# Kernel optimization log

Hardware: AMD Instinct MI355X
Metric: run time of the kernel (lower is better)

## Reference

```python
import jax, jax.numpy as jnp
import numpy as np

B, T, D, H = 4, 2048, 1024, 16
HD = D // H


def setup_inputs() -> dict:
    key = jax.random.key(0)
    ks = jax.random.split(key, 4)
    x = jax.random.normal(ks[0], (B, T, D), dtype=jnp.float32)
    # causal lower-triangular mask, broadcastable to [B, H, T, T]
    mask = jnp.tril(jnp.ones((T, T), dtype=bool))[None, None, :, :]
    w_qkv = jax.random.normal(ks[1], (D, 3 * D), dtype=jnp.float32) * (1.0 / np.sqrt(D))
    b_qkv = jnp.zeros((3 * D,), dtype=jnp.float32)
    w_out = jax.random.normal(ks[2], (D, D), dtype=jnp.float32) * (1.0 / np.sqrt(D))
    b_out = jnp.zeros((D,), dtype=jnp.float32)
    return {"x": x, "mask": mask, "w_qkv": w_qkv, "b_qkv": b_qkv,
            "w_out": w_out, "b_out": b_out}


def reference(x, mask, w_qkv, b_qkv, w_out, b_out):
    Bx, Tx, C = x.shape
    qkv = x @ w_qkv + b_qkv                       # [B, T, 3D]
    q, k, v = jnp.split(qkv, 3, axis=-1)
    # [B, T, H, hd] -> [B, H, T, hd]
    q = q.reshape(Bx, Tx, H, HD).transpose(0, 2, 1, 3)
    k = k.reshape(Bx, Tx, H, HD).transpose(0, 2, 1, 3)
    v = v.reshape(Bx, Tx, H, HD).transpose(0, 2, 1, 3)
    scale = 1.0 / np.sqrt(HD).astype(np.float32)
    att = jnp.einsum('bhqd,bhkd->bhqk', q, k) * scale   # [B, H, T, T]
    att = jnp.where(mask, att, -jnp.inf)
    att = jax.nn.softmax(att, axis=-1)
    y = jnp.einsum('bhqk,bhkd->bhqd', att, v)            # [B, H, T, hd]
    y = y.transpose(0, 2, 1, 3).reshape(Bx, Tx, C)
    return y @ w_out + b_out
```

## Files before the change

kernel.cpp:

```cpp
#include <hip/hip_runtime.h>


typedef unsigned short u16;
typedef unsigned int u32;
typedef __attribute__((ext_vector_type(8))) short short8;
typedef __attribute__((ext_vector_type(4))) float f32x4;

#define MASKV (-1e30f)
#define SCLOG 0.1803368801111444f

__device__ __forceinline__ u16 f2bf(float f) {
  union { float f; u32 u; } x; x.f = f;
  u32 r = x.u + 0x7FFFu + ((x.u >> 16) & 1u);
  return (u16)(r >> 16);
}

__device__ __forceinline__ void async16(const u16* g, u16* l) {
  __builtin_amdgcn_global_load_lds((__attribute__((address_space(1))) void*)g,
                                   (__attribute__((address_space(3))) void*)l,
                                   16, 0, 0);
}

__global__ void cvt_x_kernel(const float* __restrict__ x, u16* __restrict__ xb) {
  size_t i = ((size_t)blockIdx.x * 256 + threadIdx.x) * 4;
  float4 v = *(const float4*)(x + i);
  uint2 o;
  o.x = (u32)f2bf(v.x) | ((u32)f2bf(v.y) << 16);
  o.y = (u32)f2bf(v.z) | ((u32)f2bf(v.w) << 16);
  *(uint2*)(xb + i) = o;
}

__global__ void cvt_tr_kernel(const float* __restrict__ src, u16* __restrict__ dst,
                              int K, int N) {
  __shared__ float tile[32][33];
  int n0 = blockIdx.x * 32, k0 = blockIdx.y * 32;
  int tx = threadIdx.x & 31, ty = threadIdx.x >> 5;
  #pragma unroll
  for (int r = ty; r < 32; r += 8)
    tile[r][tx] = src[(size_t)(k0 + r) * N + n0 + tx];
  __syncthreads();
  #pragma unroll
  for (int r = ty; r < 32; r += 8)
    dst[(size_t)(n0 + r) * K + k0 + tx] = f2bf(tile[tx][r]);
}

template<bool BF16OUT>
__global__ __launch_bounds__(256) void gemm_bt(const u16* __restrict__ A,
                                               const u16* __restrict__ Bt,
                                               const float* __restrict__ bias,
                                               void* __restrict__ Cv, int N) {
  constexpr int K = 1024;
  __shared__ alignas(16) u16 As[128 * 32];
  __shared__ alignas(16) u16 Bs[128 * 32];
  const int t = threadIdx.x;
  const int w = t >> 6, lane = t & 63, quad = lane >> 4, l15 = lane & 15;
  const int m0 = blockIdx.y * 128, n0 = blockIdx.x * 128;
  const int wm = (w >> 1) * 64, wn = (w & 1) * 64;

  size_t gA[2], gB[2];
  int lds_st[2];
  #pragma unroll
  for (int ii = 0; ii < 2; ii++) {
    const int row = w * 32 + ii * 16 + (lane >> 2);
    const int db = (lane & 3) ^ (row & 3);
    gA[ii] = (size_t)(m0 + row) * K + db * 8;
    gB[ii] = (size_t)(n0 + row) * K + db * 8;
    lds_st[ii] = (w * 32 + ii * 16) * 32 + lane * 8;
  }
  const int fsw = (quad ^ (l15 & 3)) << 3;

  f32x4 acc[4][4];
  #pragma unroll
  for (int i = 0; i < 4; i++)
    #pragma unroll
    for (int j = 0; j < 4; j++)
      acc[i][j] = (f32x4){0.f, 0.f, 0.f, 0.f};

  for (int k0 = 0; k0 < K; k0 += 32) {
    __syncthreads();
    async16(A + gA[0] + k0, As + lds_st[0]);
    async16(A + gA[1] + k0, As + lds_st[1]);
    async16(Bt + gB[0] + k0, Bs + lds_st[0]);
    async16(Bt + gB[1] + k0, Bs + lds_st[1]);
    __syncthreads();
    short8 af[4], bf[4];
    #pragma unroll
    for (int i = 0; i < 4; i++)
      af[i] = *(const short8*)(As + (wm + i * 16 + l15) * 32 + fsw);
    #pragma unroll
    for (int j = 0; j < 4; j++)
      bf[j] = *(const short8*)(Bs + (wn + j * 16 + l15) * 32 + fsw);
    #pragma unroll
    for (int i = 0; i < 4; i++)
      #pragma unroll
      for (int j = 0; j < 4; j++)
        acc[i][j] = __builtin_amdgcn_mfma_f32_16x16x32_bf16(af[i], bf[j], acc[i][j], 0, 0, 0);
  }
  #pragma unroll
  for (int j = 0; j < 4; j++) {
    const int col = n0 + wn + j * 16 + l15;
    const float bv = bias[col];
    #pragma unroll
    for (int i = 0; i < 4; i++) {
      const int row = m0 + wm + i * 16 + quad * 4;
      #pragma unroll
      for (int r = 0; r < 4; r++) {
        float v = acc[i][j][r] + bv;
        if (BF16OUT) ((u16*)Cv)[(size_t)(row + r) * N + col] = f2bf(v);
        else         ((float*)Cv)[(size_t)(row + r) * N + col] = v;
      }
    }
  }
}

__global__ __launch_bounds__(256) void flash_kernel(const u16* __restrict__ qkv,
                                                    u16* __restrict__ attn) {
  constexpr int T = 2048, N3 = 3072;
  __shared__ alignas(16) u16 Ks[2][64 * 64];
  __shared__ alignas(16) u16 VsT[2][64 * 64];
  __shared__ alignas(16) u16 Ps[4][32 * 64];
  const int t = threadIdx.x;
  const int w = t >> 6, lane = t & 63, quad = lane >> 4, l15 = lane & 15;
  const int bh = blockIdx.x, b = bh >> 4, h = bh & 15;
  const u16* base = qkv + (size_t)b * T * N3 + h * 64;
  const u16* Kg = base + 1024;
  const u16* Vg = base + 2048;

  size_t gK[2];
  int ldsK[2];
  #pragma unroll
  for (int ii = 0; ii < 2; ii++) {
    const int key0 = w * 16 + ii * 8;
    const int key = key0 + (lane >> 3);
    const int db = ((lane & 7) ^ (key0 >> 3) ^ (lane >> 3)) & 7;
    gK[ii] = (size_t)key * N3 + db * 8;
    ldsK[ii] = key0 * 64 + lane * 8;
  }
  const int vkey = w * 8 + (lane >> 3);
  const int vchunk = lane & 7;
  const size_t gV = (size_t)vkey * N3 + vchunk * 8;

  short8 onesf;
  #pragma unroll
  for (int j = 0; j < 8; j++) onesf[j] = (short)0x3F80;

  #pragma unroll 1
  for (int half = 0; half < 2; half++) {
    const int qt = half ? (int)blockIdx.y : 15 - (int)blockIdx.y;
    const int q0 = qt * 128;
    const int qw = q0 + w * 32;
    const int ktmax = 2 * qt + 1;

    short8 qf[2][2];
    #pragma unroll
    for (int mi = 0; mi < 2; mi++)
      #pragma unroll
      for (int kc = 0; kc < 2; kc++)
        qf[mi][kc] = *(const short8*)(base + (size_t)(qw + mi * 16 + l15) * N3 + kc * 32 + quad * 8);

    f32x4 o[2][4], lac[2];
    #pragma unroll
    for (int mi = 0; mi < 2; mi++) {
      lac[mi] = (f32x4){0.f, 0.f, 0.f, 0.f};
      #pragma unroll
      for (int dt = 0; dt < 4; dt++) o[mi][dt] = (f32x4){0.f, 0.f, 0.f, 0.f};
    }

    async16(Kg + gK[0], &Ks[0][ldsK[0]]);
    async16(Kg + gK[1], &Ks[0][ldsK[1]]);
    {
      int4 vp0 = *(const int4*)(Vg + gV);
      int4 vp1 = *(const int4*)(Vg + gV + (size_t)32 * N3);
      union { int4 v; u16 u[8]; } uv;
      #pragma unroll
      for (int rd = 0; rd < 2; rd++) {
        uv.v = rd ? vp1 : vp0;
        const int kb = w + 4 * rd, ko = lane >> 3;
        #pragma unroll
        for (int j = 0; j < 8; j++)
          VsT[0][(vchunk * 8 + j) * 64 + (((kb ^ vchunk ^ j) & 7) << 3) + ko] = uv.u[j];
      }
    }

    int cur = 0;
    for (int kt = 0; kt <= ktmax; ++kt) {
      __syncthreads();
      const bool live = (kt * 64 <= qw + 31);
      const u16* Kc = Ks[cur];
      const u16* Vc = VsT[cur];
      short8 kf[4][2];
      if (live) {
        #pragma unroll
        for (int nt = 0; nt < 4; nt++) {
          const int kx = (nt * 2 + (l15 >> 3)) ^ (l15 & 7);
          #pragma unroll
          for (int ks = 0; ks < 2; ks++)
            kf[nt][ks] = *(const short8*)(Kc + (nt * 16 + l15) * 64 +
                                          ((((ks * 4 + quad) ^ kx) & 7) << 3));
        }
      }
      int4 vp0, vp1;
      if (kt < ktmax) {
        const size_t koff = (size_t)(kt + 1) * 64 * N3;
        async16(Kg + koff + gK[0], &Ks[cur ^ 1][ldsK[0]]);
        async16(Kg + koff + gK[1], &Ks[cur ^ 1][ldsK[1]]);
        vp0 = *(const int4*)(Vg + koff + gV);
        vp1 = *(const int4*)(Vg + koff + gV + (size_t)32 * N3);
      }
      if (live) {
        u16* pw = Ps[w];
        const bool needMask = (kt * 64 + 63 > qw);
        #pragma unroll
        for (int mi = 0; mi < 2; mi++) {
          f32x4 s[4];
          #pragma unroll
          for (int nt = 0; nt < 4; nt++) s[nt] = (f32x4){0.f, 0.f, 0.f, 0.f};
          #pragma unroll
          for (int nt = 0; nt < 4; nt++)
            #pragma unroll
            for (int kc = 0; kc < 2; kc++)
              s[nt] = __builtin_amdgcn_mfma_f32_16x16x32_bf16(qf[mi][kc], kf[nt][kc], s[nt], 0, 0, 0);
          if (needMask) {
            #pragma unroll
            for (int r = 0; r < 4; r++) {
              const int row = qw + mi * 16 + quad * 4 + r;
              #pragma unroll
              for (int nt = 0; nt < 4; nt++) {
                const int col = kt * 64 + nt * 16 + l15;
                if (col > row) s[nt][r] = MASKV;
              }
            }
          }
          #pragma unroll
          for (int nt = 0; nt < 4; nt++) {
            const int lc = nt * 2 + (l15 >> 3);
            #pragma unroll
            for (int r = 0; r < 4; r++) {
              const int rl = mi * 16 + quad * 4 + r;
              const float p = __builtin_amdgcn_exp2f(fminf(s[nt][r], 400.f) * SCLOG);
              union { float f; u32 u; } pc; pc.f = p;
              const int fp_ = (rl ^ (rl >> 1)) & 7;
              pw[rl * 64 + (((lc ^ fp_) & 7) << 3) + (l15 & 7)] = (u16)(pc.u >> 16);
            }
          }
        }
        const int fpr = (l15 ^ (l15 >> 1)) & 7;
        #pragma unroll
        for (int ks = 0; ks < 2; ks++) {
          const int cb = ks * 4 + quad;
          const int ph = (cb ^ fpr) & 7;
          short8 pf0 = *(const short8*)(pw + l15 * 64 + (ph << 3));
          short8 pf1 = *(const short8*)(pw + (16 + l15) * 64 + (ph << 3));
          #pragma unroll
          for (int dt = 0; dt < 4; dt++) {
            const int vx = (dt * 2 + (l15 >> 3)) ^ (l15 & 7);
            short8 vf = *(const short8*)(Vc + (dt * 16 + l15) * 64 + (((cb ^ vx) & 7) << 3));
            o[0][dt] = __builtin_amdgcn_mfma_f32_16x16x32_bf16(pf0, vf, o[0][dt], 0, 0, 0);
            o[1][dt] = __builtin_amdgcn_mfma_f32_16x16x32_bf16(pf1, vf, o[1][dt], 0, 0, 0);
          }
          lac[0] = __builtin_amdgcn_mfma_f32_16x16x32_bf16(pf0, onesf, lac[0], 0, 0, 0);
          lac[1] = __builtin_amdgcn_mfma_f32_16x16x32_bf16(pf1, onesf, lac[1], 0, 0, 0);
        }
      }
      if (kt < ktmax) {
        u16* Vn = (u16*)VsT[cur ^ 1];
        union { int4 v; u16 u[8]; } uv;
        #pragma unroll
        for (int rd = 0; rd < 2; rd++) {
          uv.v = rd ? vp1 : vp0;
          const int kb = w + 4 * rd, ko = lane >> 3;
          #pragma unroll
          for (int j = 0; j < 8; j++)
            Vn[(vchunk * 8 + j) * 64 + (((kb ^ vchunk ^ j) & 7) << 3) + ko] = uv.u[j];
        }
      }
      cur ^= 1;
    }

    #pragma unroll
    for (int mi = 0; mi < 2; mi++)
      #pragma unroll
      for (int r = 0; r < 4; r++) {
        const float invl = 1.0f / lac[mi][r];
        const int row = qw + mi * 16 + quad * 4 + r;
        const size_t off = (size_t)(b * T + row) * 1024 + h * 64;
        #pragma unroll
        for (int dt = 0; dt < 4; dt++)
          attn[off + dt * 16 + l15] = f2bf(o[mi][dt][r] * invl);
      }
  }
}

extern "C" void kernel_launch(void* const* d_in, const int* in_sizes, int n_in,
                              void* d_out, int out_size, void* d_ws, size_t ws_size,
                              hipStream_t stream) {
  (void)in_sizes; (void)n_in; (void)out_size; (void)ws_size;
  const float* x     = (const float*)d_in[0];
  const float* w_qkv = (const float*)d_in[2];
  const float* b_qkv = (const float*)d_in[3];
  const float* w_out = (const float*)d_in[4];
  const float* b_out = (const float*)d_in[5];
  float* out = (float*)d_out;

  char* ws = (char*)d_ws;
  u16* xb    = (u16*)(ws);
  u16* wqkvT = (u16*)(ws + 16777216);
  u16* woutT = (u16*)(ws + 23068672);
  u16* qkvb  = (u16*)(ws + 25165824);
  u16* attnb = (u16*)(ws + 75497472);

  cvt_x_kernel<<<8192, 256, 0, stream>>>(x, xb);
  cvt_tr_kernel<<<dim3(96, 32), 256, 0, stream>>>(w_qkv, wqkvT, 1024, 3072);
  cvt_tr_kernel<<<dim3(32, 32), 256, 0, stream>>>(w_out, woutT, 1024, 1024);
  gemm_bt<true ><<<dim3(24, 64), 256, 0, stream>>>(xb, wqkvT, b_qkv, qkvb, 3072);
  flash_kernel<<<dim3(64, 8), 256, 0, stream>>>(qkvb, attnb);
  gemm_bt<false><<<dim3(8, 64), 256, 0, stream>>>(attnb, woutT, b_out, out, 1024);
}
```

Measured before the change: 329.0 us.

## Pre-transpose V and rewrite flash kernel with 32x32 MFMA, register-resident P

Adds a separate kernel that writes V transposed per head into workspace, so the attention kernel reads K and V^T straight from global memory with no LDS staging or double buffering. The flash kernel now gives each wave its own 32-query strip and uses 32x32x16 MFMAs computing S^T, so P goes from registers into the PV MFMA through a cross-half shuffle instead of an LDS round trip. Row sums are accumulated in scalar registers rather than with a ones-MFMA. Each block now covers one 128-query tile on a grid twice as large, and output is staged through LDS for coalesced stores. The tradeoff is an extra launch plus a write and reread of V, and more reliance on L2 for K/V reuse across waves.

```diff
diff --git a/kernel.cpp b/kernel.cpp
--- a/kernel.cpp
+++ b/kernel.cpp
@@ -5,9 +5,10 @@
 typedef unsigned int u32;
 typedef __attribute__((ext_vector_type(8))) short short8;
 typedef __attribute__((ext_vector_type(4))) float f32x4;
-
+typedef __attribute__((ext_vector_type(16))) float f32x16;
+
+#define SCLOG 0.1803368801111444f
 #define MASKV (-1e30f)
-#define SCLOG 0.1803368801111444f
 
 __device__ __forceinline__ u16 f2bf(float f) {
   union { float f; u32 u; } x; x.f = f;
@@ -113,181 +114,148 @@
   }
 }
 
+__global__ __launch_bounds__(256) void vt_kernel(const u16* __restrict__ qkv,
+                                                 u16* __restrict__ vt) {
+  __shared__ alignas(16) u16 L[64 * 64];
+  const int t = threadIdx.x;
+  const int w = t >> 6, lane = t & 63;
+  const int bh = blockIdx.y;
+  const int b = bh >> 4, h = bh & 15;
+  const int t0 = blockIdx.x * 64;
+  const u16* Vg = qkv + (size_t)b * 2048 * 3072 + 2048 + h * 64;
+  const int vkey = w * 8 + (lane >> 3);
+  const int vchunk = lane & 7;
+  int4 v0 = *(const int4*)(Vg + (size_t)(t0 + vkey) * 3072 + vchunk * 8);
+  int4 v1 = *(const int4*)(Vg + (size_t)(t0 + vkey + 32) * 3072 + vchunk * 8);
+  union { int4 v; u16 u[8]; } uv;
+  #pragma unroll
+  for (int rd = 0; rd < 2; rd++) {
+    uv.v = rd ? v1 : v0;
+    const int kb = w + 4 * rd, ko = lane >> 3;
+    #pragma unroll
+    for (int j = 0; j < 8; j++)
+      L[(vchunk * 8 + j) * 64 + (((kb ^ vchunk ^ j) & 7) << 3) + ko] = uv.u[j];
+  }
+  __syncthreads();
+  const int d = t >> 2;
+  #pragma unroll
+  for (int gg = 0; gg < 2; gg++) {
+    const int g = (t & 3) * 2 + gg;
+    const int phys = (g ^ (d >> 3) ^ (d & 7)) & 7;
+    int4 val = *(const int4*)(L + d * 64 + phys * 8);
+    *(int4*)(vt + ((size_t)bh * 64 + d) * 2048 + t0 + g * 8) = val;
+  }
+}
+
 __global__ __launch_bounds__(256) void flash_kernel(const u16* __restrict__ qkv,
+                                                    const u16* __restrict__ vt,
                                                     u16* __restrict__ attn) {
   constexpr int T = 2048, N3 = 3072;
-  __shared__ alignas(16) u16 Ks[2][64 * 64];
-  __shared__ alignas(16) u16 VsT[2][64 * 64];
-  __shared__ alignas(16) u16 Ps[4][32 * 64];
+  __shared__ alignas(16) u16 Ob[4][32 * 64];
   const int t = threadIdx.x;
-  const int w = t >> 6, lane = t & 63, quad = lane >> 4, l15 = lane & 15;
+  const int w = t >> 6, lane = t & 63;
+  const int col = lane & 31, half = lane >> 5;
   const int bh = blockIdx.x, b = bh >> 4, h = bh & 15;
+  const int s = (15 - (int)blockIdx.y) * 4 + w;
+  const int s32 = s * 32;
   const u16* base = qkv + (size_t)b * T * N3 + h * 64;
   const u16* Kg = base + 1024;
-  const u16* Vg = base + 2048;
-
-  size_t gK[2];
-  int ldsK[2];
-  #pragma unroll
-  for (int ii = 0; ii < 2; ii++) {
-    const int key0 = w * 16 + ii * 8;
-    const int key = key0 + (lane >> 3);
-    const int db = ((lane & 7) ^ (key0 >> 3) ^ (lane >> 3)) & 7;
-    gK[ii] = (size_t)key * N3 + db * 8;
-    ldsK[ii] = key0 * 64 + lane * 8;
-  }
-  const int vkey = w * 8 + (lane >> 3);
-  const int vchunk = lane & 7;
-  const size_t gV = (size_t)vkey * N3 + vchunk * 8;
-
-  short8 onesf;
-  #pragma unroll
-  for (int j = 0; j < 8; j++) onesf[j] = (short)0x3F80;
-
-  #pragma unroll 1
-  for (int half = 0; half < 2; half++) {
-    const int qt = half ? (int)blockIdx.y : 15 - (int)blockIdx.y;
-    const int q0 = qt * 128;
-    const int qw = q0 + w * 32;
-    const int ktmax = 2 * qt + 1;
-
-    short8 qf[2][2];
-    #pragma unroll
-    for (int mi = 0; mi < 2; mi++)
-      #pragma unroll
-      for (int kc = 0; kc < 2; kc++)
-        qf[mi][kc] = *(const short8*)(base + (size_t)(qw + mi * 16 + l15) * N3 + kc * 32 + quad * 8);
-
-    f32x4 o[2][4], lac[2];
-    #pragma unroll
-    for (int mi = 0; mi < 2; mi++) {
-      lac[mi] = (f32x4){0.f, 0.f, 0.f, 0.f};
-      #pragma unroll
-      for (int dt = 0; dt < 4; dt++) o[mi][dt] = (f32x4){0.f, 0.f, 0.f, 0.f};
-    }
-
-    async16(Kg + gK[0], &Ks[0][ldsK[0]]);
-    async16(Kg + gK[1], &Ks[0][ldsK[1]]);
-    {
-      int4 vp0 = *(const int4*)(Vg + gV);
-      int4 vp1 = *(const int4*)(Vg + gV + (size_t)32 * N3);
-      union { int4 v; u16 u[8]; } uv;
-      #pragma unroll
-      for (int rd = 0; rd < 2; rd++) {
-        uv.v = rd ? vp1 : vp0;
-        const int kb = w + 4 * rd, ko = lane >> 3;
+  const u16* Vt = vt + (size_t)bh * 64 * 2048;
+
+  short8 qf[4];
+  {
+    const u16* qrow = base + (size_t)(s32 + col) * N3 + half * 8;
+    #pragma unroll
+    for (int kk = 0; kk < 4; kk++)
+      qf[kk] = *(const short8*)(qrow + kk * 16);
+  }
+
+  f32x16 o[2];
+  o[0] = (f32x16)(0.f);
+  o[1] = (f32x16)(0.f);
+  float l_acc = 0.f;
+
+  const int ntiles = (s >> 1) + 1;
+  for (int kt = 0; kt < ntiles; ++kt) {
+    #pragma unroll
+    for (int st = 0; st < 2; st++) {
+      const int keybase = kt * 64 + st * 32;
+      if (keybase > s32) break;
+      const u16* krow = Kg + (size_t)(keybase + col) * N3 + half * 8;
+      short8 kf[4];
+      #pragma unroll
+      for (int kk = 0; kk < 4; kk++)
+        kf[kk] = *(const short8*)(krow + kk * 16);
+      f32x16 S = (f32x16)(0.f);
+      #pragma unroll
+      for (int kk = 0; kk < 4; kk++)
+        S = __builtin_amdgcn_mfma_f32_32x32x16_bf16(kf[kk], qf[kk], S, 0, 0, 0);
+      union { f32x16 v; u32 u[16]; float f[16]; } su;
+      su.v = S;
+      if (keybase == s32) {
         #pragma unroll
-        for (int j = 0; j < 8; j++)
-          VsT[0][(vchunk * 8 + j) * 64 + (((kb ^ vchunk ^ j) & 7) << 3) + ko] = uv.u[j];
-      }
-    }
-
-    int cur = 0;
-    for (int kt = 0; kt <= ktmax; ++kt) {
-      __syncthreads();
-      const bool live = (kt * 64 <= qw + 31);
-      const u16* Kc = Ks[cur];
-      const u16* Vc = VsT[cur];
-      short8 kf[4][2];
-      if (live) {
+        for (int i = 0; i < 16; i++) {
+          const int kl = (i & 3) + 8 * (i >> 2) + 4 * half;
+          if (kl > col) su.f[i] = MASKV;
+        }
+      }
+      #pragma unroll
+      for (int i = 0; i < 16; i++) {
+        const float p = __builtin_amdgcn_exp2f(fminf(su.f[i], 240.f) * SCLOG);
+        union { float f; u32 u; } pc; pc.f = p;
+        su.u[i] = pc.u;
+        union { u32 u; float f; } tr; tr.u = pc.u & 0xFFFF0000u;
+        l_acc += tr.f;
+      }
+      u32 pk[8], xp[8];
+      #pragma unroll
+      for (int bq = 0; bq < 4; bq++)
         #pragma unroll
-        for (int nt = 0; nt < 4; nt++) {
-          const int kx = (nt * 2 + (l15 >> 3)) ^ (l15 & 7);
-          #pragma unroll
-          for (int ks = 0; ks < 2; ks++)
-            kf[nt][ks] = *(const short8*)(Kc + (nt * 16 + l15) * 64 +
-                                          ((((ks * 4 + quad) ^ kx) & 7) << 3));
+        for (int c = 0; c < 2; c++)
+          pk[bq * 2 + c] = __builtin_amdgcn_perm(su.u[(bq << 2) + (c << 1) + 1],
+                                                 su.u[(bq << 2) + (c << 1)], 0x07060302u);
+      #pragma unroll
+      for (int i = 0; i < 8; i++)
+        xp[i] = (u32)__shfl_xor((int)pk[i], 32, 64);
+      #pragma unroll
+      for (int cc = 0; cc < 2; cc++) {
+        union { u32 d[4]; short8 s8; } pf;
+        pf.d[0] = half ? xp[4 * cc + 2] : pk[4 * cc];
+        pf.d[1] = half ? xp[4 * cc + 3] : pk[4 * cc + 1];
+        pf.d[2] = half ? pk[4 * cc + 2] : xp[4 * cc];
+        pf.d[3] = half ? pk[4 * cc + 3] : xp[4 * cc + 1];
+        #pragma unroll
+        for (int dt = 0; dt < 2; dt++) {
+          const short8 vf = *(const short8*)(Vt + (size_t)(dt * 32 + col) * 2048 +
+                                             keybase + cc * 16 + half * 8);
+          o[dt] = __builtin_amdgcn_mfma_f32_32x32x16_bf16(vf, pf.s8, o[dt], 0, 0, 0);
         }
       }
-      int4 vp0, vp1;
-      if (kt < ktmax) {
-        const size_t koff = (size_t)(kt + 1) * 64 * N3;
-        async16(Kg + koff + gK[0], &Ks[cur ^ 1][ldsK[0]]);
-        async16(Kg + koff + gK[1], &Ks[cur ^ 1][ldsK[1]]);
-        vp0 = *(const int4*)(Vg + koff + gV);
-        vp1 = *(const int4*)(Vg + koff + gV + (size_t)32 * N3);
-      }
-      if (live) {
-        u16* pw = Ps[w];
-        const bool needMask = (kt * 64 + 63 > qw);
-        #pragma unroll
-        for (int mi = 0; mi < 2; mi++) {
-          f32x4 s[4];
-          #pragma unroll
-          for (int nt = 0; nt < 4; nt++) s[nt] = (f32x4){0.f, 0.f, 0.f, 0.f};
-          #pragma unroll
-          for (int nt = 0; nt < 4; nt++)
-            #pragma unroll
-            for (int kc = 0; kc < 2; kc++)
-              s[nt] = __builtin_amdgcn_mfma_f32_16x16x32_bf16(qf[mi][kc], kf[nt][kc], s[nt], 0, 0, 0);
-          if (needMask) {
-            #pragma unroll
-            for (int r = 0; r < 4; r++) {
-              const int row = qw + mi * 16 + quad * 4 + r;
-              #pragma unroll
-              for (int nt = 0; nt < 4; nt++) {
-                const int col = kt * 64 + nt * 16 + l15;
-                if (col > row) s[nt][r] = MASKV;
-              }
-            }
-          }
-          #pragma unroll
-          for (int nt = 0; nt < 4; nt++) {
-            const int lc = nt * 2 + (l15 >> 3);
-            #pragma unroll
-            for (int r = 0; r < 4; r++) {
-              const int rl = mi * 16 + quad * 4 + r;
-              const float p = __builtin_amdgcn_exp2f(fminf(s[nt][r], 400.f) * SCLOG);
-              union { float f; u32 u; } pc; pc.f = p;
-              const int fp_ = (rl ^ (rl >> 1)) & 7;
-              pw[rl * 64 + (((lc ^ fp_) & 7) << 3) + (l15 & 7)] = (u16)(pc.u >> 16);
-            }
-          }
-        }
-        const int fpr = (l15 ^ (l15 >> 1)) & 7;
-        #pragma unroll
-        for (int ks = 0; ks < 2; ks++) {
-          const int cb = ks * 4 + quad;
-          const int ph = (cb ^ fpr) & 7;
-          short8 pf0 = *(const short8*)(pw + l15 * 64 + (ph << 3));
-          short8 pf1 = *(const short8*)(pw + (16 + l15) * 64 + (ph << 3));
-          #pragma unroll
-          for (int dt = 0; dt < 4; dt++) {
-            const int vx = (dt * 2 + (l15 >> 3)) ^ (l15 & 7);
-            short8 vf = *(const short8*)(Vc + (dt * 16 + l15) * 64 + (((cb ^ vx) & 7) << 3));
-            o[0][dt] = __builtin_amdgcn_mfma_f32_16x16x32_bf16(pf0, vf, o[0][dt], 0, 0, 0);
-            o[1][dt] = __builtin_amdgcn_mfma_f32_16x16x32_bf16(pf1, vf, o[1][dt], 0, 0, 0);
-          }
-          lac[0] = __builtin_amdgcn_mfma_f32_16x16x32_bf16(pf0, onesf, lac[0], 0, 0, 0);
-          lac[1] = __builtin_amdgcn_mfma_f32_16x16x32_bf16(pf1, onesf, lac[1], 0, 0, 0);
-        }
-      }
-      if (kt < ktmax) {
-        u16* Vn = (u16*)VsT[cur ^ 1];
-        union { int4 v; u16 u[8]; } uv;
-        #pragma unroll
-        for (int rd = 0; rd < 2; rd++) {
-          uv.v = rd ? vp1 : vp0;
-          const int kb = w + 4 * rd, ko = lane >> 3;
-          #pragma unroll
-          for (int j = 0; j < 8; j++)
-            Vn[(vchunk * 8 + j) * 64 + (((kb ^ vchunk ^ j) & 7) << 3) + ko] = uv.u[j];
-        }
-      }
-      cur ^= 1;
-    }
-
-    #pragma unroll
-    for (int mi = 0; mi < 2; mi++)
-      #pragma unroll
-      for (int r = 0; r < 4; r++) {
-        const float invl = 1.0f / lac[mi][r];
-        const int row = qw + mi * 16 + quad * 4 + r;
-        const size_t off = (size_t)(b * T + row) * 1024 + h * 64;
-        #pragma unroll
-        for (int dt = 0; dt < 4; dt++)
-          attn[off + dt * 16 + l15] = f2bf(o[mi][dt][r] * invl);
-      }
+    }
+  }
+
+  const float l_tot = l_acc + (float)__shfl_xor(l_acc, 32, 64);
+  const float inv = 1.0f / l_tot;
+
+  u16* buf = Ob[w];
+  #pragma unroll
+  for (int dt = 0; dt < 2; dt++)
+    #pragma unroll
+    for (int i = 0; i < 16; i++) {
+      const int d = dt * 32 + (i & 3) + 8 * (i >> 2) + 4 * half;
+      buf[col * 64 + ((((d >> 3) ^ (col & 7)) & 7) << 3) + (d & 7)] = f2bf(o[dt][i] * inv);
+    }
+  __syncthreads();
+  {
+    const int qr = lane >> 1;
+    const size_t orow = (size_t)(b * T + s32 + qr) * 1024 + h * 64;
+    #pragma unroll
+    for (int ccs = 0; ccs < 4; ccs++) {
+      const int c = (lane & 1) * 4 + ccs;
+      const int phys = (c ^ (qr & 7)) & 7;
+      int4 val = *(const int4*)(buf + qr * 64 + phys * 8);
+      *(int4*)(attn + orow + c * 8) = val;
+    }
   }
 }
 
@@ -307,12 +275,14 @@
   u16* wqkvT = (u16*)(ws + 16777216);
   u16* woutT = (u16*)(ws + 23068672);
   u16* qkvb  = (u16*)(ws + 25165824);
-  u16* attnb = (u16*)(ws + 75497472);
+  u16* vtb   = (u16*)(ws + 75497472);
+  u16* attnb = xb;
 
   cvt_x_kernel<<<8192, 256, 0, stream>>>(x, xb);
   cvt_tr_kernel<<<dim3(96, 32), 256, 0, stream>>>(w_qkv, wqkvT, 1024, 3072);
   cvt_tr_kernel<<<dim3(32, 32), 256, 0, stream>>>(w_out, woutT, 1024, 1024);
   gemm_bt<true ><<<dim3(24, 64), 256, 0, stream>>>(xb, wqkvT, b_qkv, qkvb, 3072);
-  flash_kernel<<<dim3(64, 8), 256, 0, stream>>>(qkvb, attnb);
+  vt_kernel<<<dim3(32, 64), 256, 0, stream>>>(qkvb, vtb);
+  flash_kernel<<<dim3(64, 16), 256, 0, stream>>>(qkvb, vtb, attnb);
   gemm_bt<false><<<dim3(8, 64), 256, 0, stream>>>(attnb, woutT, b_out, out, 1024);
 }
```

Result: slower. 354.2 us (+7.7%).

## Split flash attention into 64-row query tiles with one block per tile

Applied to the files above, without the earlier changes.

The flash kernel goes from 512 blocks, each handling two paired 128-row query tiles (a long and a short one, for causal balance), to 2048 blocks that each handle one 64-row tile, with 16 rows per wave. This raises parallelism and occupancy through smaller per-thread register and LDS footprints, and removes the per-wave dead-tile 'live' checks. The cost is reloading each K/V tile for more query tiles, which doubles K/V traffic, and relying on the scheduler to balance uneven causal work. The attention output buffer now reuses the x bf16 workspace, and the exp clamp is lowered.

```diff
diff --git a/kernel.cpp b/kernel.cpp
--- a/kernel.cpp
+++ b/kernel.cpp
@@ -118,10 +118,13 @@
   constexpr int T = 2048, N3 = 3072;
   __shared__ alignas(16) u16 Ks[2][64 * 64];
   __shared__ alignas(16) u16 VsT[2][64 * 64];
-  __shared__ alignas(16) u16 Ps[4][32 * 64];
+  __shared__ alignas(16) u16 Ps[4][16 * 64];
   const int t = threadIdx.x;
   const int w = t >> 6, lane = t & 63, quad = lane >> 4, l15 = lane & 15;
   const int bh = blockIdx.x, b = bh >> 4, h = bh & 15;
+  const int qt = 31 - (int)blockIdx.y;
+  const int qw = qt * 64 + w * 16;
+
   const u16* base = qkv + (size_t)b * T * N3 + h * 64;
   const u16* Kg = base + 1024;
   const u16* Vg = base + 2048;
@@ -144,33 +147,104 @@
   #pragma unroll
   for (int j = 0; j < 8; j++) onesf[j] = (short)0x3F80;
 
-  #pragma unroll 1
-  for (int half = 0; half < 2; half++) {
-    const int qt = half ? (int)blockIdx.y : 15 - (int)blockIdx.y;
-    const int q0 = qt * 128;
-    const int qw = q0 + w * 32;
-    const int ktmax = 2 * qt + 1;
-
-    short8 qf[2][2];
-    #pragma unroll
-    for (int mi = 0; mi < 2; mi++)
+  short8 qf[2];
+  #pragma unroll
+  for (int kc = 0; kc < 2; kc++)
+    qf[kc] = *(const short8*)(base + (size_t)(qw + l15) * N3 + kc * 32 + quad * 8);
+
+  f32x4 o[4], lac;
+  lac = (f32x4){0.f, 0.f, 0.f, 0.f};
+  #pragma unroll
+  for (int dt = 0; dt < 4; dt++) o[dt] = (f32x4){0.f, 0.f, 0.f, 0.f};
+
+  async16(Kg + gK[0], &Ks[0][ldsK[0]]);
+  async16(Kg + gK[1], &Ks[0][ldsK[1]]);
+  {
+    int4 vp0 = *(const int4*)(Vg + gV);
+    int4 vp1 = *(const int4*)(Vg + gV + (size_t)32 * N3);
+    union { int4 v; u16 u[8]; } uv;
+    #pragma unroll
+    for (int rd = 0; rd < 2; rd++) {
+      uv.v = rd ? vp1 : vp0;
+      const int kb = w + 4 * rd, ko = lane >> 3;
+      #pragma unroll
+      for (int j = 0; j < 8; j++)
+        VsT[0][(vchunk * 8 + j) * 64 + (((kb ^ vchunk ^ j) & 7) << 3) + ko] = uv.u[j];
+    }
+  }
+
+  int cur = 0;
+  for (int kt = 0; kt <= qt; ++kt) {
+    __syncthreads();
+    const u16* Kc = Ks[cur];
+    const u16* Vc = VsT[cur];
+    u16* pw = Ps[w];
+    short8 kf[4][2];
+    #pragma unroll
+    for (int nt = 0; nt < 4; nt++) {
+      const int kx = (nt * 2 + (l15 >> 3)) ^ (l15 & 7);
+      #pragma unroll
+      for (int ks = 0; ks < 2; ks++)
+        kf[nt][ks] = *(const short8*)(Kc + (nt * 16 + l15) * 64 +
+                                      ((((ks * 4 + quad) ^ kx) & 7) << 3));
+    }
+    int4 vp0, vp1;
+    if (kt < qt) {
+      const size_t koff = (size_t)(kt + 1) * 64 * N3;
+      async16(Kg + koff + gK[0], &Ks[cur ^ 1][ldsK[0]]);
+      async16(Kg + koff + gK[1], &Ks[cur ^ 1][ldsK[1]]);
+      vp0 = *(const int4*)(Vg + koff + gV);
+      vp1 = *(const int4*)(Vg + koff + gV + (size_t)32 * N3);
+    }
+
+    f32x4 s[4];
+    #pragma unroll
+    for (int nt = 0; nt < 4; nt++) s[nt] = (f32x4){0.f, 0.f, 0.f, 0.f};
+    #pragma unroll
+    for (int nt = 0; nt < 4; nt++)
       #pragma unroll
       for (int kc = 0; kc < 2; kc++)
-        qf[mi][kc] = *(const short8*)(base + (size_t)(qw + mi * 16 + l15) * N3 + kc * 32 + quad * 8);
-
-    f32x4 o[2][4], lac[2];
-    #pragma unroll
-    for (int mi = 0; mi < 2; mi++) {
-      lac[mi] = (f32x4){0.f, 0.f, 0.f, 0.f};
-      #pragma unroll
-      for (int dt = 0; dt < 4; dt++) o[mi][dt] = (f32x4){0.f, 0.f, 0.f, 0.f};
-    }
-
-    async16(Kg + gK[0], &Ks[0][ldsK[0]]);
-    async16(Kg + gK[1], &Ks[0][ldsK[1]]);
-    {
-      int4 vp0 = *(const int4*)(Vg + gV);
-      int4 vp1 = *(const int4*)(Vg + gV + (size_t)32 * N3);
+        s[nt] = __builtin_amdgcn_mfma_f32_16x16x32_bf16(qf[kc], kf[nt][kc], s[nt], 0, 0, 0);
+
+    if (kt == qt) {
+      #pragma unroll
+      for (int r = 0; r < 4; r++) {
+        const int row = qw + quad * 4 + r;
+        #pragma unroll
+        for (int nt = 0; nt < 4; nt++) {
+          const int col = kt * 64 + nt * 16 + l15;
+          if (col > row) s[nt][r] = MASKV;
+        }
+      }
+    }
+    #pragma unroll
+    for (int nt = 0; nt < 4; nt++) {
+      const int lc = nt * 2 + (l15 >> 3);
+      #pragma unroll
+      for (int r = 0; r < 4; r++) {
+        const int rl = quad * 4 + r;
+        const float p = __builtin_amdgcn_exp2f(fminf(s[nt][r], 240.f) * SCLOG);
+        union { float f; u32 u; } pc; pc.f = p;
+        const int fp_ = (rl ^ (rl >> 1)) & 7;
+        pw[rl * 64 + (((lc ^ fp_) & 7) << 3) + (l15 & 7)] = (u16)(pc.u >> 16);
+      }
+    }
+    const int fpr = (l15 ^ (l15 >> 1)) & 7;
+    #pragma unroll
+    for (int ks = 0; ks < 2; ks++) {
+      const int cb = ks * 4 + quad;
+      short8 pf = *(const short8*)(pw + l15 * 64 + (((cb ^ fpr) & 7) << 3));
+      #pragma unroll
+      for (int dt = 0; dt < 4; dt++) {
+        const int vx = (dt * 2 + (l15 >> 3)) ^ (l15 & 7);
+        short8 vf = *(const short8*)(Vc + (dt * 16 + l15) * 64 + (((cb ^ vx) & 7) << 3));
+        o[dt] = __builtin_amdgcn_mfma_f32_16x16x32_bf16(pf, vf, o[dt], 0, 0, 0);
+      }
+      lac = __builtin_amdgcn_mfma_f32_16x16x32_bf16(pf, onesf, lac, 0, 0, 0);
+    }
+
+    if (kt < qt) {
+      u16* Vn = (u16*)VsT[cur ^ 1];
       union { int4 v; u16 u[8]; } uv;
       #pragma unroll
       for (int rd = 0; rd < 2; rd++) {
@@ -178,116 +252,20 @@
         const int kb = w + 4 * rd, ko = lane >> 3;
         #pragma unroll
         for (int j = 0; j < 8; j++)
-          VsT[0][(vchunk * 8 + j) * 64 + (((kb ^ vchunk ^ j) & 7) << 3) + ko] = uv.u[j];
-      }
-    }
-
-    int cur = 0;
-    for (int kt = 0; kt <= ktmax; ++kt) {
-      __syncthreads();
-      const bool live = (kt * 64 <= qw + 31);
-      const u16* Kc = Ks[cur];
-      const u16* Vc = VsT[cur];
-      short8 kf[4][2];
-      if (live) {
-        #pragma unroll
-        for (int nt = 0; nt < 4; nt++) {
-          const int kx = (nt * 2 + (l15 >> 3)) ^ (l15 & 7);
-          #pragma unroll
-          for (int ks = 0; ks < 2; ks++)
-            kf[nt][ks] = *(const short8*)(Kc + (nt * 16 + l15) * 64 +
-                                          ((((ks * 4 + quad) ^ kx) & 7) << 3));
-        }
-      }
-      int4 vp0, vp1;
-      if (kt < ktmax) {
-        const size_t koff = (size_t)(kt + 1) * 64 * N3;
-        async16(Kg + koff + gK[0], &Ks[cur ^ 1][ldsK[0]]);
-        async16(Kg + koff + gK[1], &Ks[cur ^ 1][ldsK[1]]);
-        vp0 = *(const int4*)(Vg + koff + gV);
-        vp1 = *(const int4*)(Vg + koff + gV + (size_t)32 * N3);
-      }
-      if (live) {
-        u16* pw = Ps[w];
-        const bool needMask = (kt * 64 + 63 > qw);
-        #pragma unroll
-        for (int mi = 0; mi < 2; mi++) {
-          f32x4 s[4];
-          #pragma unroll
-          for (int nt = 0; nt < 4; nt++) s[nt] = (f32x4){0.f, 0.f, 0.f, 0.f};
-          #pragma unroll
-          for (int nt = 0; nt < 4; nt++)
-            #pragma unroll
-            for (int kc = 0; kc < 2; kc++)
-              s[nt] = __builtin_amdgcn_mfma_f32_16x16x32_bf16(qf[mi][kc], kf[nt][kc], s[nt], 0, 0, 0);
-          if (needMask) {
-            #pragma unroll
-            for (int r = 0; r < 4; r++) {
-              const int row = qw + mi * 16 + quad * 4 + r;
-              #pragma unroll
-              for (int nt = 0; nt < 4; nt++) {
-                const int col = kt * 64 + nt * 16 + l15;
-                if (col > row) s[nt][r] = MASKV;
-              }
-            }
-          }
-          #pragma unroll
-          for (int nt = 0; nt < 4; nt++) {
-            const int lc = nt * 2 + (l15 >> 3);
-            #pragma unroll
-            for (int r = 0; r < 4; r++) {
-              const int rl = mi * 16 + quad * 4 + r;
-              const float p = __builtin_amdgcn_exp2f(fminf(s[nt][r], 400.f) * SCLOG);
-              union { float f; u32 u; } pc; pc.f = p;
-              const int fp_ = (rl ^ (rl >> 1)) & 7;
-              pw[rl * 64 + (((lc ^ fp_) & 7) << 3) + (l15 & 7)] = (u16)(pc.u >> 16);
-            }
-          }
-        }
-        const int fpr = (l15 ^ (l15 >> 1)) & 7;
-        #pragma unroll
-        for (int ks = 0; ks < 2; ks++) {
-          const int cb = ks * 4 + quad;
-          const int ph = (cb ^ fpr) & 7;
-          short8 pf0 = *(const short8*)(pw + l15 * 64 + (ph << 3));
-          short8 pf1 = *(const short8*)(pw + (16 + l15) * 64 + (ph << 3));
-          #pragma unroll
-          for (int dt = 0; dt < 4; dt++) {
-            const int vx = (dt * 2 + (l15 >> 3)) ^ (l15 & 7);
-            short8 vf = *(const short8*)(Vc + (dt * 16 + l15) * 64 + (((cb ^ vx) & 7) << 3));
-            o[0][dt] = __builtin_amdgcn_mfma_f32_16x16x32_bf16(pf0, vf, o[0][dt], 0, 0, 0);
-            o[1][dt] = __builtin_amdgcn_mfma_f32_16x16x32_bf16(pf1, vf, o[1][dt], 0, 0, 0);
-          }
-          lac[0] = __builtin_amdgcn_mfma_f32_16x16x32_bf16(pf0, onesf, lac[0], 0, 0, 0);
-          lac[1] = __builtin_amdgcn_mfma_f32_16x16x32_bf16(pf1, onesf, lac[1], 0, 0, 0);
-        }
-      }
-      if (kt < ktmax) {
-        u16* Vn = (u16*)VsT[cur ^ 1];
-        union { int4 v; u16 u[8]; } uv;
-        #pragma unroll
-        for (int rd = 0; rd < 2; rd++) {
-          uv.v = rd ? vp1 : vp0;
-          const int kb = w + 4 * rd, ko = lane >> 3;
-          #pragma unroll
-          for (int j = 0; j < 8; j++)
-            Vn[(vchunk * 8 + j) * 64 + (((kb ^ vchunk ^ j) & 7) << 3) + ko] = uv.u[j];
-        }
-      }
-      cur ^= 1;
-    }
-
-    #pragma unroll
-    for (int mi = 0; mi < 2; mi++)
-      #pragma unroll
-      for (int r = 0; r < 4; r++) {
-        const float invl = 1.0f / lac[mi][r];
-        const int row = qw + mi * 16 + quad * 4 + r;
-        const size_t off = (size_t)(b * T + row) * 1024 + h * 64;
-        #pragma unroll
-        for (int dt = 0; dt < 4; dt++)
-          attn[off + dt * 16 + l15] = f2bf(o[mi][dt][r] * invl);
-      }
+          Vn[(vchunk * 8 + j) * 64 + (((kb ^ vchunk ^ j) & 7) << 3) + ko] = uv.u[j];
+      }
+    }
+    cur ^= 1;
+  }
+
+  #pragma unroll
+  for (int r = 0; r < 4; r++) {
+    const float invl = 1.0f / lac[r];
+    const int row = qw + quad * 4 + r;
+    const size_t off = (size_t)(b * T + row) * 1024 + h * 64;
+    #pragma unroll
+    for (int dt = 0; dt < 4; dt++)
+      attn[off + dt * 16 + l15] = f2bf(o[dt][r] * invl);
   }
 }
 
@@ -307,12 +285,12 @@
   u16* wqkvT = (u16*)(ws + 16777216);
   u16* woutT = (u16*)(ws + 23068672);
   u16* qkvb  = (u16*)(ws + 25165824);
-  u16* attnb = (u16*)(ws + 75497472);
+  u16* attnb = xb;
 
   cvt_x_kernel<<<8192, 256, 0, stream>>>(x, xb);
   cvt_tr_kernel<<<dim3(96, 32), 256, 0, stream>>>(w_qkv, wqkvT, 1024, 3072);
   cvt_tr_kernel<<<dim3(32, 32), 256, 0, stream>>>(w_out, woutT, 1024, 1024);
   gemm_bt<true ><<<dim3(24, 64), 256, 0, stream>>>(xb, wqkvT, b_qkv, qkvb, 3072);
-  flash_kernel<<<dim3(64, 8), 256, 0, stream>>>(qkvb, attnb);
+  flash_kernel<<<dim3(64, 32), 256, 0, stream>>>(qkvb, attnb);
   gemm_bt<false><<<dim3(8, 64), 256, 0, stream>>>(attnb, woutT, b_out, out, 1024);
 }
```

Measured after the change: 289.1 us. 1.14x faster.
